# Optimization experiments

Hardware: AMD Instinct MI355X
Metric: run time of the kernel (lower is better)

## Reference

```python
import jax, jax.numpy as jnp
import numpy as np
from jax.ops import segment_sum

N = 100000
E = 1600000
D_IN = 64
D_H = 64
D_OUT = 16


def _gcn_norm(edge_index, n_nodes):
    # PyG GCNConv default: add self-loops, symmetric normalization.
    src, dst = edge_index[0], edge_index[1]
    loop = jnp.arange(n_nodes, dtype=edge_index.dtype)
    src = jnp.concatenate([src, loop])
    dst = jnp.concatenate([dst, loop])
    deg = segment_sum(jnp.ones(src.shape[0], dtype=jnp.float32), dst, num_segments=n_nodes)
    dinv = jnp.where(deg > 0, jax.lax.rsqrt(deg), 0.0)
    norm = dinv[src] * dinv[dst]  # [E + N]
    return src, dst, norm


def _gcn_layer(x, W, b, src, dst, norm, n_nodes):
    h = x @ W  # dense transform first (out_channels <= in_channels)
    msg = h[src] * norm[:, None]          # gather + scale  [E+N, out]
    agg = segment_sum(msg, dst, num_segments=n_nodes)  # scatter-add
    return agg + b


def setup_inputs() -> dict:
    key = jax.random.key(0)
    ks = jax.random.split(key, 10)
    x = jax.random.normal(ks[0], (N, D_IN), dtype=jnp.float32)
    edge_index = jax.random.randint(ks[1], (2, E), 0, N, dtype=jnp.int64)

    def glorot(k, fan_in, fan_out):
        lim = np.sqrt(6.0 / (fan_in + fan_out)).astype(np.float32)
        return jax.random.uniform(k, (fan_in, fan_out), jnp.float32, -lim, lim)

    return {
        "x": x,
        "edge_index": edge_index,
        "W1": glorot(ks[2], D_IN, D_H), "b1": jnp.zeros((D_H,), jnp.float32),
        "W2": glorot(ks[3], D_H, D_H), "b2": jnp.zeros((D_H,), jnp.float32),
        "W3": glorot(ks[4], D_H, D_H), "b3": jnp.zeros((D_H,), jnp.float32),
        "W4": glorot(ks[5], D_H, D_OUT), "b4": jnp.zeros((D_OUT,), jnp.float32),
    }


def reference(x, edge_index, W1, b1, W2, b2, W3, b3, W4, b4):
    n = x.shape[0]
    src, dst, norm = _gcn_norm(edge_index, n)
    h = jax.nn.relu(_gcn_layer(x, W1, b1, src, dst, norm, n))
    h = jax.nn.relu(_gcn_layer(h, W2, b2, src, dst, norm, n))
    h = jax.nn.relu(_gcn_layer(h, W3, b3, src, dst, norm, n))
    return _gcn_layer(h, W4, b4, src, dst, norm, n)
```

## Files before the change

kernel.cpp:

```cpp
#include <hip/hip_runtime.h>
#include <hip/hip_fp16.h>

#define NN 100000
#define NE 1600000
#define BK 512
#define BKSH 9
#define NBKT 196
#define SLOT 9216
#define SRCMASK 0x1FFFF

typedef _Float16 half2v __attribute__((ext_vector_type(2)));

__device__ inline float dot2acc(unsigned int a, unsigned int b, float c) {
#if __has_builtin(__builtin_amdgcn_fdot2)
    union { unsigned int u; half2v h; } ua, ub;
    ua.u = a; ub.u = b;
    return __builtin_amdgcn_fdot2(ua.h, ub.h, c, false);
#else
    float2 fa = __half22float2(*(const __half2*)&a);
    float2 fb = __half22float2(*(const __half2*)&b);
    return c + fa.x * fb.x + fa.y * fb.y;
#endif
}

__device__ inline int wave_incl_scan(int v, int lane) {
#pragma unroll
    for (int off = 1; off < 64; off <<= 1) {
        int t = __shfl_up(v, off, 64);
        if (lane >= off) v += t;
    }
    return v;
}


__global__ __launch_bounds__(256) void zero_small_kernel(int* __restrict__ p, int n) {
    int i = threadIdx.x + blockIdx.x * 256;
    if (i < n) p[i] = 0;
}

__global__ __launch_bounds__(512) void bscatter_kernel(const int* __restrict__ src,
                                                       const int* __restrict__ dst,
                                                       int* __restrict__ bcur,
                                                       unsigned int* __restrict__ bedges,
                                                       int e) {
    __shared__ int h[8][256];
    __shared__ int tot[256];
    __shared__ int sc[256];
    __shared__ int gb[256];
    __shared__ int2 stg[4096];
    int tid = threadIdx.x, wv = tid >> 6;
    int tile = blockIdx.x * 4096;
    int cnt_tile = min(4096, e - tile);
    for (int i = tid; i < 8 * 256; i += 512) ((int*)h)[i] = 0;
    __syncthreads();
    unsigned int pk[8]; int rk[8], bk[8];
#pragma unroll
    for (int j = 0; j < 8; j++) {
        int li = tid + j * 512;
        if (li < cnt_tile) {
            int s = src[tile + li];
            int d = dst[tile + li];
            bk[j] = d >> BKSH;
            pk[j] = ((unsigned)(d & (BK - 1)) << 17) | (unsigned)s;
            rk[j] = atomicAdd(&h[wv][bk[j]], 1);
        } else bk[j] = -1;
    }
    __syncthreads();
    if (tid < 256) {
        int run = 0;
#pragma unroll
        for (int w = 0; w < 8; w++) { int c = h[w][tid]; h[w][tid] = run; run += c; }
        tot[tid] = run;
    }
    __syncthreads();
    if (tid < 64) {
        int b0 = tid * 4;
        int c0 = tot[b0], c1 = tot[b0 + 1], c2 = tot[b0 + 2], c3 = tot[b0 + 3];
        int s4 = c0 + c1 + c2 + c3;
        int incl = wave_incl_scan(s4, tid);
        int base = incl - s4;
        sc[b0] = base; sc[b0 + 1] = base + c0;
        sc[b0 + 2] = base + c0 + c1; sc[b0 + 3] = base + c0 + c1 + c2;
        if (c0) gb[b0] = atomicAdd(&bcur[b0], c0);
        if (c1) gb[b0 + 1] = atomicAdd(&bcur[b0 + 1], c1);
        if (c2) gb[b0 + 2] = atomicAdd(&bcur[b0 + 2], c2);
        if (c3) gb[b0 + 3] = atomicAdd(&bcur[b0 + 3], c3);
    }
    __syncthreads();
#pragma unroll
    for (int j = 0; j < 8; j++)
        if (bk[j] >= 0) stg[sc[bk[j]] + h[wv][bk[j]] + rk[j]] = make_int2((int)pk[j], bk[j]);
    __syncthreads();
#pragma unroll
    for (int j = 0; j < 8; j++) {
        int li = tid + j * 512;
        if (li < cnt_tile) {
            int2 p2 = stg[li];
            int b = p2.y;
            bedges[(size_t)b * SLOT + gb[b] + (li - sc[b])] = (unsigned int)p2.x;
        }
    }
}

__global__ __launch_bounds__(1024) void bfill_kernel(const unsigned int* __restrict__ bedges,
                                                     const int* __restrict__ bcur,
                                                     const float* __restrict__ x,
                                                     int* __restrict__ start,
                                                     int* __restrict__ cnt,
                                                     float* __restrict__ dinv,
                                                     int* __restrict__ csr,
                                                     __half* __restrict__ g0) {
    __shared__ int sub[4][BK];
    __shared__ int lcnt[BK];
    __shared__ int lstart[BK];
    int q = blockIdx.x, tid = threadIdx.x;
    int grp = (tid >> 6) >> 2;
    size_t ebase = (size_t)q * SLOT;
    int ec = bcur[q];
    int nbase = q * BK;
    for (int i = tid; i < 4 * BK; i += 1024) ((int*)sub)[i] = 0;
    __syncthreads();
    unsigned int pk[9]; int rk[9];
    int nit = 0;
    for (int i = tid; i < ec; i += 1024) {
        pk[nit] = __builtin_nontemporal_load(&bedges[ebase + i]);
        rk[nit] = atomicAdd(&sub[grp][pk[nit] >> 17], 1);
        nit++;
    }
    __syncthreads();
    if (tid < BK) {
        int run = 0;
#pragma unroll
        for (int g = 0; g < 4; g++) { int c = sub[g][tid]; sub[g][tid] = run; run += c; }
        lcnt[tid] = run;
    }
    __syncthreads();
    if (tid < 64) {
        int b0 = tid * 8;
        int c[8]; int s = 0;
#pragma unroll
        for (int k = 0; k < 8; k++) { c[k] = lcnt[b0 + k]; s += c[k]; }
        int incl = wave_incl_scan(s, tid);
        int run = incl - s;
#pragma unroll
        for (int k = 0; k < 8; k++) { lstart[b0 + k] = run; run += c[k]; }
    }
    __syncthreads();
    if (tid < BK) {
        int nd = nbase + tid;
        if (nd < NN) {
            start[nd] = (int)ebase + lstart[tid];
            cnt[nd]   = lcnt[tid];
            dinv[nd]  = rsqrtf((float)lcnt[tid] + 1.0f);
        }
    }
    for (int it = 0, i = tid; it < nit; it++, i += 1024) {
        int d = pk[it] >> 17;
        csr[ebase + lstart[d] + sub[grp][d] + rk[it]] = (int)(pk[it] & SRCMASK);
    }
    for (int i = tid; i < BK * 16; i += 1024) {
        int l = i >> 4, c4 = (i & 15) * 4;
        int nd = nbase + l;
        if (nd < NN) {
            float dv = rsqrtf((float)lcnt[l] + 1.0f);
            float4 v = *(const float4*)&x[(size_t)nd * 64 + c4];
            __half2 h01 = __floats2half2_rn(v.x * dv, v.y * dv);
            __half2 h23 = __floats2half2_rn(v.z * dv, v.w * dv);
            __half2* gp = (__half2*)&g0[(size_t)nd * 64 + c4];
            gp[0] = h01;
            gp[1] = h23;
        }
    }
}

__global__ __launch_bounds__(512) void fused_layer_kernel(const __half* __restrict__ g,
                                                          const int* __restrict__ csr,
                                                          const int* __restrict__ start,
                                                          const int* __restrict__ cnt,
                                                          const float* __restrict__ dinv,
                                                          const float* __restrict__ Wg,
                                                          const float* __restrict__ bias,
                                                          __half* __restrict__ gout, int n) {
    __shared__ uint4 wpk[8][64];
    __shared__ __half zh[8][64];
    __shared__ float bs[64];
    int tid = threadIdx.x;
    {
        int p = tid >> 6, c = tid & 63;
        float w[8];
#pragma unroll
        for (int i = 0; i < 8; i++) w[i] = Wg[(8 * p + i) * 64 + c];
        union { __half2 h; unsigned int u; } u0, u1, u2, u3;
        u0.h = __floats2half2_rn(w[0], w[1]);
        u1.h = __floats2half2_rn(w[2], w[3]);
        u2.h = __floats2half2_rn(w[4], w[5]);
        u3.h = __floats2half2_rn(w[6], w[7]);
        wpk[p][c] = make_uint4(u0.u, u1.u, u2.u, u3.u);
    }
    if (tid < 64) bs[tid] = bias[tid];
    __syncthreads();

    int wv = tid >> 6, lane = tid & 63;
    int node = blockIdx.x * 8 + wv;
    float acc = 0.f;
    float dv = 0.f;
    if (node < n) {
        int st = __builtin_amdgcn_readfirstlane(start[node]);
        int cn = __builtin_amdgcn_readfirstlane(cnt[node]);
        dv = dinv[node];
        acc = __half2float(g[(size_t)node * 64 + lane]);
        int e = 0;
        for (; e + 7 < cn; e += 8) {
            int u[8]; float a[8];
#pragma unroll
            for (int j = 0; j < 8; j++) u[j] = __builtin_nontemporal_load(&csr[st + e + j]);
#pragma unroll
            for (int j = 0; j < 8; j++) a[j] = __half2float(g[(size_t)u[j] * 64 + lane]);
            acc += ((a[0] + a[1]) + (a[2] + a[3])) + ((a[4] + a[5]) + (a[6] + a[7]));
        }
        for (; e + 3 < cn; e += 4) {
            int u0 = __builtin_nontemporal_load(&csr[st + e + 0]);
            int u1 = __builtin_nontemporal_load(&csr[st + e + 1]);
            int u2 = __builtin_nontemporal_load(&csr[st + e + 2]);
            int u3 = __builtin_nontemporal_load(&csr[st + e + 3]);
            float a0 = __half2float(g[(size_t)u0 * 64 + lane]);
            float a1 = __half2float(g[(size_t)u1 * 64 + lane]);
            float a2 = __half2float(g[(size_t)u2 * 64 + lane]);
            float a3 = __half2float(g[(size_t)u3 * 64 + lane]);
            acc += (a0 + a1) + (a2 + a3);
        }
        for (; e < cn; e++) {
            int u = __builtin_nontemporal_load(&csr[st + e]);
            acc += __half2float(g[(size_t)u * 64 + lane]);
        }
    }
    zh[wv][lane] = __float2half_rn(acc);
    if (node < n) {
        float t = 0.f;
#pragma unroll
        for (int p = 0; p < 8; p++) {
            uint4 wq = wpk[p][lane];
            uint4 zq = *(const uint4*)&zh[wv][p * 8];
            t = dot2acc(zq.x, wq.x, t);
            t = dot2acc(zq.y, wq.y, t);
            t = dot2acc(zq.z, wq.z, t);
            t = dot2acc(zq.w, wq.w, t);
        }
        float o = dv * t + bs[lane];
        o = fmaxf(o, 0.f);
        gout[(size_t)node * 64 + lane] = __float2half_rn(dv * o);
    }
}

__global__ __launch_bounds__(128) void gemm16_kernel(const __half* __restrict__ xin,
                                                     const float* __restrict__ W,
                                                     __half* __restrict__ s, int n) {
    constexpr int DOUT = 16;
    constexpr int ROWS = 128;
    __shared__ float xs[ROWS][65];
    __shared__ float ws[64][DOUT];
    int tid = threadIdx.x;
    int row0 = blockIdx.x * ROWS;
    for (int i = tid; i < 64 * DOUT; i += 128) ws[i / DOUT][i % DOUT] = W[i];
    for (int i = tid; i < ROWS * 16; i += 128) {
        int r = i >> 4, c = (i & 15) * 4;
        float4 v = make_float4(0.f, 0.f, 0.f, 0.f);
        if (row0 + r < n) {
            const __half* hp = xin + (size_t)(row0 + r) * 64 + c;
            float2 f01 = __half22float2(*(const __half2*)hp);
            float2 f23 = __half22float2(*(const __half2*)(hp + 2));
            v = make_float4(f01.x, f01.y, f23.x, f23.y);
        }
        xs[r][c] = v.x; xs[r][c + 1] = v.y; xs[r][c + 2] = v.z; xs[r][c + 3] = v.w;
    }
    __syncthreads();
    int rbase = tid;
    float acc[16];
#pragma unroll
    for (int j = 0; j < 16; j++) acc[j] = 0.f;
    for (int k = 0; k < 64; k++) {
        float xv = xs[rbase][k];
#pragma unroll
        for (int j = 0; j < 4; j++) {
            float4 wv = *(const float4*)&ws[k][j * 4];
            acc[j * 4 + 0] += xv * wv.x;
            acc[j * 4 + 1] += xv * wv.y;
            acc[j * 4 + 2] += xv * wv.z;
            acc[j * 4 + 3] += xv * wv.w;
        }
    }
    int r = row0 + rbase;
    if (r < n) {
        union { ushort u[16]; uint4 q[2]; } pk;
#pragma unroll
        for (int j = 0; j < 16; j++)
            pk.u[j] = __half_as_ushort(__float2half_rn(acc[j]));
        uint4* sp = (uint4*)&s[(size_t)r * DOUT];
        sp[0] = pk.q[0];
        sp[1] = pk.q[1];
    }
}

__global__ __launch_bounds__(256) void agg16_kernel(const __half* __restrict__ s,
                                                    const int* __restrict__ csr,
                                                    const int* __restrict__ start,
                                                    const int* __restrict__ cnt,
                                                    const float* __restrict__ dinv,
                                                    const float* __restrict__ bias,
                                                    float* __restrict__ out, int n) {
    constexpr int D = 16;
    int tid = threadIdx.x;
    int lane = tid & 63;
    int wave = tid >> 6;
    int col = lane % D;
    int grp = lane / D;
    int node = (blockIdx.x * 4 + wave) * 4 + grp;
    if (node >= n) return;
    int st = start[node];
    int cn = cnt[node];
    float acc = __half2float(s[(size_t)node * D + col]);
    int e = 0;
    for (; e + 7 < cn; e += 8) {
        int u[8]; float a[8];
#pragma unroll
        for (int j = 0; j < 8; j++) u[j] = __builtin_nontemporal_load(&csr[st + e + j]);
#pragma unroll
        for (int j = 0; j < 8; j++) a[j] = __half2float(s[(size_t)u[j] * D + col]);
        acc += ((a[0] + a[1]) + (a[2] + a[3])) + ((a[4] + a[5]) + (a[6] + a[7]));
    }
    for (; e + 3 < cn; e += 4) {
        int u0 = __builtin_nontemporal_load(&csr[st + e + 0]);
        int u1 = __builtin_nontemporal_load(&csr[st + e + 1]);
        int u2 = __builtin_nontemporal_load(&csr[st + e + 2]);
        int u3 = __builtin_nontemporal_load(&csr[st + e + 3]);
        float a0 = __half2float(s[(size_t)u0 * D + col]);
        float a1 = __half2float(s[(size_t)u1 * D + col]);
        float a2 = __half2float(s[(size_t)u2 * D + col]);
        float a3 = __half2float(s[(size_t)u3 * D + col]);
        acc += (a0 + a1) + (a2 + a3);
    }
    for (; e < cn; e++) {
        int u = __builtin_nontemporal_load(&csr[st + e]);
        acc += __half2float(s[(size_t)u * D + col]);
    }
    float o = dinv[node] * acc + bias[col];
    __builtin_nontemporal_store(o, out + (size_t)node * D + col);
}


extern "C" void kernel_launch(void* const* d_in, const int* in_sizes, int n_in,
                              void* d_out, int out_size, void* d_ws, size_t ws_size,
                              hipStream_t stream) {
    const float* x  = (const float*)d_in[0];
    const int* ei   = (const int*)d_in[1];
    const float* W1 = (const float*)d_in[2];
    const float* b1 = (const float*)d_in[3];
    const float* W2 = (const float*)d_in[4];
    const float* b2 = (const float*)d_in[5];
    const float* W3 = (const float*)d_in[6];
    const float* b3 = (const float*)d_in[7];
    const float* W4 = (const float*)d_in[8];
    const float* b4 = (const float*)d_in[9];
    const int* src = ei;
    const int* dst = ei + NE;

    char* w = (char*)d_ws;
    auto alloc = [&](size_t bytes) {
        char* p = w;
        w += (bytes + 127) & ~(size_t)127;
        return p;
    };
    float* dinv  = (float*)alloc((size_t)NN * 4);
    int* cnt     = (int*)alloc((size_t)NN * 4);
    int* start   = (int*)alloc((size_t)NN * 4);
    int* bcur    = (int*)alloc(256 * 4);
    int* csr     = (int*)alloc((size_t)NBKT * SLOT * 4);
    __half* gA   = (__half*)alloc((size_t)NN * 64 * 2);
    __half* gB   = (__half*)alloc((size_t)NN * 64 * 2);
    __half* s4   = (__half*)alloc((size_t)NN * 16 * 2);
    unsigned int* bedges = (unsigned int*)alloc((size_t)NBKT * SLOT * 4);

    zero_small_kernel<<<1, 256, 0, stream>>>(bcur, 256);
    bscatter_kernel<<<(NE + 4095) / 4096, 512, 0, stream>>>(src, dst, bcur, bedges, NE);
    bfill_kernel<<<NBKT, 1024, 0, stream>>>(bedges, bcur, x, start, cnt, dinv, csr, gA);

    const int FB = (NN + 7) / 8;
    fused_layer_kernel<<<FB, 512, 0, stream>>>(gA, csr, start, cnt, dinv, W1, b1, gB, NN);
    fused_layer_kernel<<<FB, 512, 0, stream>>>(gB, csr, start, cnt, dinv, W2, b2, gA, NN);
    fused_layer_kernel<<<FB, 512, 0, stream>>>(gA, csr, start, cnt, dinv, W3, b3, gB, NN);

    const int GB = (NN + 127) / 128;
    const int AB16 = (NN + 15) / 16;
    gemm16_kernel<<<GB, 128, 0, stream>>>(gB, W4, s4, NN);
    agg16_kernel<<<AB16, 256, 0, stream>>>(s4, csr, start, cnt, dinv, b4, (float*)d_out, NN);
}
```

Measured before the change: 340.2 us.

## Fuse final 64x16 GEMM into layer-3 kernel and restructure last aggregation

Layer 3's fused kernel now multiplies its activated output by W4 in-register via fp16 dot products and writes the 16-wide result directly. This removes the separate gemm16 kernel and its read/write of the 64-wide fp16 intermediate. The final aggregation switches to one node per wave, with four edges handled in parallel per wave and combined by cross-lane shuffle reduction. Nontemporal hints on CSR loads are also dropped. The fusion adds some fp16 rounding of the layer-3 output before the W4 product.

```diff
diff --git a/kernel.cpp b/kernel.cpp
--- a/kernel.cpp
+++ b/kernel.cpp
@@ -173,6 +173,7 @@
     }
 }
 
+template <bool EMIT16>
 __global__ __launch_bounds__(512) void fused_layer_kernel(const __half* __restrict__ g,
                                                           const int* __restrict__ csr,
                                                           const int* __restrict__ start,
@@ -180,8 +181,10 @@
                                                           const float* __restrict__ dinv,
                                                           const float* __restrict__ Wg,
                                                           const float* __restrict__ bias,
+                                                          const float* __restrict__ W4g,
                                                           __half* __restrict__ gout, int n) {
     __shared__ uint4 wpk[8][64];
+    __shared__ uint4 w4pk[8][16];
     __shared__ __half zh[8][64];
     __shared__ float bs[64];
     int tid = threadIdx.x;
@@ -196,6 +199,18 @@
         u2.h = __floats2half2_rn(w[4], w[5]);
         u3.h = __floats2half2_rn(w[6], w[7]);
         wpk[p][c] = make_uint4(u0.u, u1.u, u2.u, u3.u);
+    }
+    if (EMIT16 && tid < 128) {
+        int p = tid >> 4, c = tid & 15;
+        float w[8];
+#pragma unroll
+        for (int i = 0; i < 8; i++) w[i] = W4g[(8 * p + i) * 16 + c];
+        union { __half2 h; unsigned int u; } u0, u1, u2, u3;
+        u0.h = __floats2half2_rn(w[0], w[1]);
+        u1.h = __floats2half2_rn(w[2], w[3]);
+        u2.h = __floats2half2_rn(w[4], w[5]);
+        u3.h = __floats2half2_rn(w[6], w[7]);
+        w4pk[p][c] = make_uint4(u0.u, u1.u, u2.u, u3.u);
     }
     if (tid < 64) bs[tid] = bias[tid];
     __syncthreads();
@@ -213,16 +228,16 @@
         for (; e + 7 < cn; e += 8) {
             int u[8]; float a[8];
 #pragma unroll
-            for (int j = 0; j < 8; j++) u[j] = __builtin_nontemporal_load(&csr[st + e + j]);
+            for (int j = 0; j < 8; j++) u[j] = csr[st + e + j];
 #pragma unroll
             for (int j = 0; j < 8; j++) a[j] = __half2float(g[(size_t)u[j] * 64 + lane]);
             acc += ((a[0] + a[1]) + (a[2] + a[3])) + ((a[4] + a[5]) + (a[6] + a[7]));
         }
         for (; e + 3 < cn; e += 4) {
-            int u0 = __builtin_nontemporal_load(&csr[st + e + 0]);
-            int u1 = __builtin_nontemporal_load(&csr[st + e + 1]);
-            int u2 = __builtin_nontemporal_load(&csr[st + e + 2]);
-            int u3 = __builtin_nontemporal_load(&csr[st + e + 3]);
+            int u0 = csr[st + e + 0];
+            int u1 = csr[st + e + 1];
+            int u2 = csr[st + e + 2];
+            int u3 = csr[st + e + 3];
             float a0 = __half2float(g[(size_t)u0 * 64 + lane]);
             float a1 = __half2float(g[(size_t)u1 * 64 + lane]);
             float a2 = __half2float(g[(size_t)u2 * 64 + lane]);
@@ -230,7 +245,7 @@
             acc += (a0 + a1) + (a2 + a3);
         }
         for (; e < cn; e++) {
-            int u = __builtin_nontemporal_load(&csr[st + e]);
+            int u = csr[st + e];
             acc += __half2float(g[(size_t)u * 64 + lane]);
         }
     }
@@ -248,56 +263,30 @@
         }
         float o = dv * t + bs[lane];
         o = fmaxf(o, 0.f);
-        gout[(size_t)node * 64 + lane] = __float2half_rn(dv * o);
-    }
-}
-
-__global__ __launch_bounds__(128) void gemm16_kernel(const __half* __restrict__ xin,
-                                                     const float* __restrict__ W,
-                                                     __half* __restrict__ s, int n) {
-    constexpr int DOUT = 16;
-    constexpr int ROWS = 128;
-    __shared__ float xs[ROWS][65];
-    __shared__ float ws[64][DOUT];
-    int tid = threadIdx.x;
-    int row0 = blockIdx.x * ROWS;
-    for (int i = tid; i < 64 * DOUT; i += 128) ws[i / DOUT][i % DOUT] = W[i];
-    for (int i = tid; i < ROWS * 16; i += 128) {
-        int r = i >> 4, c = (i & 15) * 4;
-        float4 v = make_float4(0.f, 0.f, 0.f, 0.f);
-        if (row0 + r < n) {
-            const __half* hp = xin + (size_t)(row0 + r) * 64 + c;
-            float2 f01 = __half22float2(*(const __half2*)hp);
-            float2 f23 = __half22float2(*(const __half2*)(hp + 2));
-            v = make_float4(f01.x, f01.y, f23.x, f23.y);
-        }
-        xs[r][c] = v.x; xs[r][c + 1] = v.y; xs[r][c + 2] = v.z; xs[r][c + 3] = v.w;
-    }
-    __syncthreads();
-    int rbase = tid;
-    float acc[16];
-#pragma unroll
-    for (int j = 0; j < 16; j++) acc[j] = 0.f;
-    for (int k = 0; k < 64; k++) {
-        float xv = xs[rbase][k];
-#pragma unroll
-        for (int j = 0; j < 4; j++) {
-            float4 wv = *(const float4*)&ws[k][j * 4];
-            acc[j * 4 + 0] += xv * wv.x;
-            acc[j * 4 + 1] += xv * wv.y;
-            acc[j * 4 + 2] += xv * wv.z;
-            acc[j * 4 + 3] += xv * wv.w;
-        }
-    }
-    int r = row0 + rbase;
-    if (r < n) {
-        union { ushort u[16]; uint4 q[2]; } pk;
-#pragma unroll
-        for (int j = 0; j < 16; j++)
-            pk.u[j] = __half_as_ushort(__float2half_rn(acc[j]));
-        uint4* sp = (uint4*)&s[(size_t)r * DOUT];
-        sp[0] = pk.q[0];
-        sp[1] = pk.q[1];
+        float g3v = dv * o;
+        if constexpr (!EMIT16) {
+            gout[(size_t)node * 64 + lane] = __float2half_rn(g3v);
+        } else {
+            zh[wv][lane] = __float2half_rn(g3v);
+            int grp = lane >> 4, c = lane & 15;
+            uint4 wq0 = w4pk[2 * grp][c];
+            uint4 wq1 = w4pk[2 * grp + 1][c];
+            uint4 zq0 = *(const uint4*)&zh[wv][grp * 16];
+            uint4 zq1 = *(const uint4*)&zh[wv][grp * 16 + 8];
+            float t4 = 0.f;
+            t4 = dot2acc(zq0.x, wq0.x, t4);
+            t4 = dot2acc(zq0.y, wq0.y, t4);
+            t4 = dot2acc(zq0.z, wq0.z, t4);
+            t4 = dot2acc(zq0.w, wq0.w, t4);
+            t4 = dot2acc(zq1.x, wq1.x, t4);
+            t4 = dot2acc(zq1.y, wq1.y, t4);
+            t4 = dot2acc(zq1.z, wq1.z, t4);
+            t4 = dot2acc(zq1.w, wq1.w, t4);
+            t4 += __shfl_xor(t4, 16, 64);
+            t4 += __shfl_xor(t4, 32, 64);
+            if (lane < 16)
+                gout[(size_t)node * 16 + lane] = __float2half_rn(t4);
+        }
     }
 }
 
@@ -308,43 +297,38 @@
                                                     const float* __restrict__ dinv,
                                                     const float* __restrict__ bias,
                                                     float* __restrict__ out, int n) {
-    constexpr int D = 16;
     int tid = threadIdx.x;
     int lane = tid & 63;
     int wave = tid >> 6;
-    int col = lane % D;
-    int grp = lane / D;
-    int node = (blockIdx.x * 4 + wave) * 4 + grp;
+    int node = blockIdx.x * 4 + wave;
     if (node >= n) return;
-    int st = start[node];
-    int cn = cnt[node];
-    float acc = __half2float(s[(size_t)node * D + col]);
-    int e = 0;
-    for (; e + 7 < cn; e += 8) {
-        int u[8]; float a[8];
-#pragma unroll
-        for (int j = 0; j < 8; j++) u[j] = __builtin_nontemporal_load(&csr[st + e + j]);
-#pragma unroll
-        for (int j = 0; j < 8; j++) a[j] = __half2float(s[(size_t)u[j] * D + col]);
-        acc += ((a[0] + a[1]) + (a[2] + a[3])) + ((a[4] + a[5]) + (a[6] + a[7]));
-    }
-    for (; e + 3 < cn; e += 4) {
-        int u0 = __builtin_nontemporal_load(&csr[st + e + 0]);
-        int u1 = __builtin_nontemporal_load(&csr[st + e + 1]);
-        int u2 = __builtin_nontemporal_load(&csr[st + e + 2]);
-        int u3 = __builtin_nontemporal_load(&csr[st + e + 3]);
-        float a0 = __half2float(s[(size_t)u0 * D + col]);
-        float a1 = __half2float(s[(size_t)u1 * D + col]);
-        float a2 = __half2float(s[(size_t)u2 * D + col]);
-        float a3 = __half2float(s[(size_t)u3 * D + col]);
-        acc += (a0 + a1) + (a2 + a3);
-    }
-    for (; e < cn; e++) {
-        int u = __builtin_nontemporal_load(&csr[st + e]);
-        acc += __half2float(s[(size_t)u * D + col]);
-    }
-    float o = dinv[node] * acc + bias[col];
-    __builtin_nontemporal_store(o, out + (size_t)node * D + col);
+    int st = __builtin_amdgcn_readfirstlane(start[node]);
+    int cn = __builtin_amdgcn_readfirstlane(cnt[node]);
+    int e4 = lane >> 4, c = lane & 15;
+    float acc = 0.f;
+    int base = 0;
+    for (; base + 7 < cn; base += 8) {
+        int ua = csr[st + base + e4];
+        int ub = csr[st + base + 4 + e4];
+        float a = __half2float(s[(size_t)ua * 16 + c]);
+        float b = __half2float(s[(size_t)ub * 16 + c]);
+        acc += a + b;
+    }
+    for (; base < cn; base += 4) {
+        float a = 0.f;
+        if (base + e4 < cn) {
+            int u = csr[st + base + e4];
+            a = __half2float(s[(size_t)u * 16 + c]);
+        }
+        acc += a;
+    }
+    acc += __shfl_xor(acc, 16, 64);
+    acc += __shfl_xor(acc, 32, 64);
+    if (lane < 16) {
+        acc += __half2float(s[(size_t)node * 16 + c]);
+        float o = dinv[node] * acc + bias[c];
+        out[(size_t)node * 16 + c] = o;
+    }
 }
 
 
@@ -385,12 +369,10 @@
     bfill_kernel<<<NBKT, 1024, 0, stream>>>(bedges, bcur, x, start, cnt, dinv, csr, gA);
 
     const int FB = (NN + 7) / 8;
-    fused_layer_kernel<<<FB, 512, 0, stream>>>(gA, csr, start, cnt, dinv, W1, b1, gB, NN);
-    fused_layer_kernel<<<FB, 512, 0, stream>>>(gB, csr, start, cnt, dinv, W2, b2, gA, NN);
-    fused_layer_kernel<<<FB, 512, 0, stream>>>(gA, csr, start, cnt, dinv, W3, b3, gB, NN);
-
-    const int GB = (NN + 127) / 128;
-    const int AB16 = (NN + 15) / 16;
-    gemm16_kernel<<<GB, 128, 0, stream>>>(gB, W4, s4, NN);
+    fused_layer_kernel<false><<<FB, 512, 0, stream>>>(gA, csr, start, cnt, dinv, W1, b1, nullptr, gB, NN);
+    fused_layer_kernel<false><<<FB, 512, 0, stream>>>(gB, csr, start, cnt, dinv, W2, b2, nullptr, gA, NN);
+    fused_layer_kernel<true><<<FB, 512, 0, stream>>>(gA, csr, start, cnt, dinv, W3, b3, W4, s4, NN);
+
+    const int AB16 = (NN + 3) / 4;
     agg16_kernel<<<AB16, 256, 0, stream>>>(s4, csr, start, cnt, dinv, b4, (float*)d_out, NN);
 }
```

Result: no change. 346.2 us (+1.8%).

## Fuse final layer into aggregate-then-transform kernel with fp16 dot products

Applied to the files above, without the earlier changes.

Replaces the separate 64→16 GEMM kernel and 16-wide aggregation kernel with a single kernel. It aggregates 64-wide fp16 neighbor rows per node, then applies W4 via packed fp16 dot2 with cross-lane shuffles. This removes one launch and the intermediate s4 buffer write and read. In exchange, each edge gather now reads 64-wide rows instead of 16-wide ones, which raises gather traffic.

```diff
diff --git a/kernel.cpp b/kernel.cpp
--- a/kernel.cpp
+++ b/kernel.cpp
@@ -252,99 +252,88 @@
     }
 }
 
-__global__ __launch_bounds__(128) void gemm16_kernel(const __half* __restrict__ xin,
-                                                     const float* __restrict__ W,
-                                                     __half* __restrict__ s, int n) {
-    constexpr int DOUT = 16;
-    constexpr int ROWS = 128;
-    __shared__ float xs[ROWS][65];
-    __shared__ float ws[64][DOUT];
+__global__ __launch_bounds__(512) void fused_out_kernel(const __half* __restrict__ g,
+                                                        const int* __restrict__ csr,
+                                                        const int* __restrict__ start,
+                                                        const int* __restrict__ cnt,
+                                                        const float* __restrict__ dinv,
+                                                        const float* __restrict__ W4g,
+                                                        const float* __restrict__ bias,
+                                                        float* __restrict__ out, int n) {
+    __shared__ uint4 w4pk[8][16];
+    __shared__ __half zh[8][64];
+    __shared__ float bs[16];
     int tid = threadIdx.x;
-    int row0 = blockIdx.x * ROWS;
-    for (int i = tid; i < 64 * DOUT; i += 128) ws[i / DOUT][i % DOUT] = W[i];
-    for (int i = tid; i < ROWS * 16; i += 128) {
-        int r = i >> 4, c = (i & 15) * 4;
-        float4 v = make_float4(0.f, 0.f, 0.f, 0.f);
-        if (row0 + r < n) {
-            const __half* hp = xin + (size_t)(row0 + r) * 64 + c;
-            float2 f01 = __half22float2(*(const __half2*)hp);
-            float2 f23 = __half22float2(*(const __half2*)(hp + 2));
-            v = make_float4(f01.x, f01.y, f23.x, f23.y);
-        }
-        xs[r][c] = v.x; xs[r][c + 1] = v.y; xs[r][c + 2] = v.z; xs[r][c + 3] = v.w;
-    }
-    __syncthreads();
-    int rbase = tid;
-    float acc[16];
-#pragma unroll
-    for (int j = 0; j < 16; j++) acc[j] = 0.f;
-    for (int k = 0; k < 64; k++) {
-        float xv = xs[rbase][k];
-#pragma unroll
-        for (int j = 0; j < 4; j++) {
-            float4 wv = *(const float4*)&ws[k][j * 4];
-            acc[j * 4 + 0] += xv * wv.x;
-            acc[j * 4 + 1] += xv * wv.y;
-            acc[j * 4 + 2] += xv * wv.z;
-            acc[j * 4 + 3] += xv * wv.w;
-        }
-    }
-    int r = row0 + rbase;
-    if (r < n) {
-        union { ushort u[16]; uint4 q[2]; } pk;
-#pragma unroll
-        for (int j = 0; j < 16; j++)
-            pk.u[j] = __half_as_ushort(__float2half_rn(acc[j]));
-        uint4* sp = (uint4*)&s[(size_t)r * DOUT];
-        sp[0] = pk.q[0];
-        sp[1] = pk.q[1];
-    }
-}
-
-__global__ __launch_bounds__(256) void agg16_kernel(const __half* __restrict__ s,
-                                                    const int* __restrict__ csr,
-                                                    const int* __restrict__ start,
-                                                    const int* __restrict__ cnt,
-                                                    const float* __restrict__ dinv,
-                                                    const float* __restrict__ bias,
-                                                    float* __restrict__ out, int n) {
-    constexpr int D = 16;
-    int tid = threadIdx.x;
-    int lane = tid & 63;
-    int wave = tid >> 6;
-    int col = lane % D;
-    int grp = lane / D;
-    int node = (blockIdx.x * 4 + wave) * 4 + grp;
-    if (node >= n) return;
-    int st = start[node];
-    int cn = cnt[node];
-    float acc = __half2float(s[(size_t)node * D + col]);
-    int e = 0;
-    for (; e + 7 < cn; e += 8) {
-        int u[8]; float a[8];
-#pragma unroll
-        for (int j = 0; j < 8; j++) u[j] = __builtin_nontemporal_load(&csr[st + e + j]);
-#pragma unroll
-        for (int j = 0; j < 8; j++) a[j] = __half2float(s[(size_t)u[j] * D + col]);
-        acc += ((a[0] + a[1]) + (a[2] + a[3])) + ((a[4] + a[5]) + (a[6] + a[7]));
-    }
-    for (; e + 3 < cn; e += 4) {
-        int u0 = __builtin_nontemporal_load(&csr[st + e + 0]);
-        int u1 = __builtin_nontemporal_load(&csr[st + e + 1]);
-        int u2 = __builtin_nontemporal_load(&csr[st + e + 2]);
-        int u3 = __builtin_nontemporal_load(&csr[st + e + 3]);
-        float a0 = __half2float(s[(size_t)u0 * D + col]);
-        float a1 = __half2float(s[(size_t)u1 * D + col]);
-        float a2 = __half2float(s[(size_t)u2 * D + col]);
-        float a3 = __half2float(s[(size_t)u3 * D + col]);
-        acc += (a0 + a1) + (a2 + a3);
-    }
-    for (; e < cn; e++) {
-        int u = __builtin_nontemporal_load(&csr[st + e]);
-        acc += __half2float(s[(size_t)u * D + col]);
-    }
-    float o = dinv[node] * acc + bias[col];
-    __builtin_nontemporal_store(o, out + (size_t)node * D + col);
+    if (tid < 128) {
+        int p = tid >> 4, c = tid & 15;
+        float w[8];
+#pragma unroll
+        for (int i = 0; i < 8; i++) w[i] = W4g[(8 * p + i) * 16 + c];
+        union { __half2 h; unsigned int u; } u0, u1, u2, u3;
+        u0.h = __floats2half2_rn(w[0], w[1]);
+        u1.h = __floats2half2_rn(w[2], w[3]);
+        u2.h = __floats2half2_rn(w[4], w[5]);
+        u3.h = __floats2half2_rn(w[6], w[7]);
+        w4pk[p][c] = make_uint4(u0.u, u1.u, u2.u, u3.u);
+    }
+    if (tid < 16) bs[tid] = bias[tid];
+    __syncthreads();
+
+    int wv = tid >> 6, lane = tid & 63;
+    int node = blockIdx.x * 8 + wv;
+    float acc = 0.f;
+    float dv = 0.f;
+    if (node < n) {
+        int st = __builtin_amdgcn_readfirstlane(start[node]);
+        int cn = __builtin_amdgcn_readfirstlane(cnt[node]);
+        dv = dinv[node];
+        acc = __half2float(g[(size_t)node * 64 + lane]);
+        int e = 0;
+        for (; e + 7 < cn; e += 8) {
+            int u[8]; float a[8];
+#pragma unroll
+            for (int j = 0; j < 8; j++) u[j] = __builtin_nontemporal_load(&csr[st + e + j]);
+#pragma unroll
+            for (int j = 0; j < 8; j++) a[j] = __half2float(g[(size_t)u[j] * 64 + lane]);
+            acc += ((a[0] + a[1]) + (a[2] + a[3])) + ((a[4] + a[5]) + (a[6] + a[7]));
+        }
+        for (; e + 3 < cn; e += 4) {
+            int u0 = __builtin_nontemporal_load(&csr[st + e + 0]);
+            int u1 = __builtin_nontemporal_load(&csr[st + e + 1]);
+            int u2 = __builtin_nontemporal_load(&csr[st + e + 2]);
+            int u3 = __builtin_nontemporal_load(&csr[st + e + 3]);
+            float a0 = __half2float(g[(size_t)u0 * 64 + lane]);
+            float a1 = __half2float(g[(size_t)u1 * 64 + lane]);
+            float a2 = __half2float(g[(size_t)u2 * 64 + lane]);
+            float a3 = __half2float(g[(size_t)u3 * 64 + lane]);
+            acc += (a0 + a1) + (a2 + a3);
+        }
+        for (; e < cn; e++) {
+            int u = __builtin_nontemporal_load(&csr[st + e]);
+            acc += __half2float(g[(size_t)u * 64 + lane]);
+        }
+    }
+    zh[wv][lane] = __float2half_rn(acc);
+    if (node < n) {
+        int p = lane >> 4, c = lane & 15;
+        uint4 wq0 = w4pk[2 * p][c];
+        uint4 wq1 = w4pk[2 * p + 1][c];
+        uint4 zq0 = *(const uint4*)&zh[wv][p * 16];
+        uint4 zq1 = *(const uint4*)&zh[wv][p * 16 + 8];
+        float t = 0.f;
+        t = dot2acc(zq0.x, wq0.x, t);
+        t = dot2acc(zq0.y, wq0.y, t);
+        t = dot2acc(zq0.z, wq0.z, t);
+        t = dot2acc(zq0.w, wq0.w, t);
+        t = dot2acc(zq1.x, wq1.x, t);
+        t = dot2acc(zq1.y, wq1.y, t);
+        t = dot2acc(zq1.z, wq1.z, t);
+        t = dot2acc(zq1.w, wq1.w, t);
+        t += __shfl_xor(t, 16, 64);
+        t += __shfl_xor(t, 32, 64);
+        if (lane < 16)
+            out[(size_t)node * 16 + lane] = dv * t + bs[lane];
+    }
 }
 
 
@@ -377,7 +366,6 @@
     int* csr     = (int*)alloc((size_t)NBKT * SLOT * 4);
     __half* gA   = (__half*)alloc((size_t)NN * 64 * 2);
     __half* gB   = (__half*)alloc((size_t)NN * 64 * 2);
-    __half* s4   = (__half*)alloc((size_t)NN * 16 * 2);
     unsigned int* bedges = (unsigned int*)alloc((size_t)NBKT * SLOT * 4);
 
     zero_small_kernel<<<1, 256, 0, stream>>>(bcur, 256);
@@ -388,9 +376,5 @@
     fused_layer_kernel<<<FB, 512, 0, stream>>>(gA, csr, start, cnt, dinv, W1, b1, gB, NN);
     fused_layer_kernel<<<FB, 512, 0, stream>>>(gB, csr, start, cnt, dinv, W2, b2, gA, NN);
     fused_layer_kernel<<<FB, 512, 0, stream>>>(gA, csr, start, cnt, dinv, W3, b3, gB, NN);
-
-    const int GB = (NN + 127) / 128;
-    const int AB16 = (NN + 15) / 16;
-    gemm16_kernel<<<GB, 128, 0, stream>>>(gB, W4, s4, NN);
-    agg16_kernel<<<AB16, 256, 0, stream>>>(s4, csr, start, cnt, dinv, b4, (float*)d_out, NN);
-}
+    fused_out_kernel<<<FB, 512, 0, stream>>>(gB, csr, start, cnt, dinv, W4, b4, (float*)d_out, NN);
+}
```

New measurement: 352.7 us. 1.04x slower.
